# Kernel optimization log

Hardware: AMD Instinct MI355X
Metric: run time of the kernel (lower is better)

The kernel has to match this reference:

```python
import jax, jax.numpy as jnp
import numpy as np

G, N, E = 4, 50000, 800000
F_IN, HID, OUT = 64, 128, 64


def setup_inputs() -> dict:
    key = jax.random.key(0)
    ks = jax.random.split(key, 4)
    x = jax.random.normal(ks[0], (G, N, F_IN), dtype=jnp.float32)
    edge_index = jax.random.randint(ks[1], (G, 2, E), 0, N)
    W1 = jax.random.normal(ks[2], (G, F_IN, HID), dtype=jnp.float32) / np.sqrt(F_IN).astype(np.float32)
    b1 = jnp.zeros((G, HID), dtype=jnp.float32)
    W2 = jax.random.normal(ks[3], (G, HID, OUT), dtype=jnp.float32) / np.sqrt(HID).astype(np.float32)
    b2 = jnp.zeros((G, OUT), dtype=jnp.float32)
    return {"x": x, "edge_index": edge_index, "W1": W1, "b1": b1, "W2": W2, "b2": b2}


def gcn_conv(x, src, dst, W, b):
    # PyG GCNConv: add self loops, symmetric norm D^-1/2 (A+I) D^-1/2, then XW + b
    n = x.shape[0]
    loop = jnp.arange(n)
    s = jnp.concatenate([src, loop])  # [E+N]
    d = jnp.concatenate([dst, loop])
    deg = jax.ops.segment_sum(jnp.ones_like(s, dtype=x.dtype), d, num_segments=n)
    dinv = jax.lax.rsqrt(deg)  # deg >= 1 because of self loops
    norm = dinv[s] * dinv[d]  # [E+N]
    h = x @ W  # [N, F_out]
    msg = h[s] * norm[:, None]  # edge-wise gather (memory-bound)
    out = jax.ops.segment_sum(msg, d, num_segments=n)  # scatter-add
    return out + b


def reference(x, edge_index, W1, b1, W2, b2):
    def per_graph(xg, eg, w1, b1g, w2, b2g):
        src, dst = eg[0], eg[1]
        h = jax.nn.elu(gcn_conv(xg, src, dst, w1, b1g))
        h = jax.nn.elu(gcn_conv(h, src, dst, w2, b2g))
        return h  # [N, OUT]

    out = jax.vmap(per_graph)(x, edge_index, W1, b1, W2, b2)  # [G, N, OUT]
    return out.reshape(G * N, OUT)  # torch.cat over graphs along dim 0
```

## Files before the change

kernel.cpp:

```cpp
#include <hip/hip_runtime.h>
#include <cstdint>

constexpr int G = 4, N = 50000, E = 800000;
constexpr int FIN = 64, HID = 128, FOUT = 64;
constexpr int NB = (N + 1023) / 1024;

constexpr int PB = 64;
constexpr int CP = E / PB;
constexpr int NBK = (N + 255) / 256;

typedef unsigned short ushort;
typedef _Float16 f16;

__device__ __forceinline__ ushort f2h(float f) {
  f16 h = (f16)f;
  return __builtin_bit_cast(ushort, h);
}
__device__ __forceinline__ float h2f(ushort u) {
  f16 h = __builtin_bit_cast(f16, u);
  return (float)h;
}

__device__ __forceinline__ void xcd_map(int b, int& g, int& chunk) {
  int xcd = b & 7;
  int sub = b >> 3;
  g = xcd >> 1;
  chunk = (xcd & 1) * 6250 + sub;
}

__global__ void k_x2h(const float4* __restrict__ X, const float* __restrict__ dinv,
                      ushort4* __restrict__ Xh, int n4) {
  int i = blockIdx.x * blockDim.x + threadIdx.x;
  if (i >= n4) return;
  float sc = dinv[i >> 4];
  float4 v = X[i];
  ushort4 o = {f2h(sc * v.x), f2h(sc * v.y), f2h(sc * v.z), f2h(sc * v.w)};
  Xh[i] = o;
}


__global__ __launch_bounds__(256) void k_phist(const int* __restrict__ ei,
                                               int* __restrict__ PH) {
  __shared__ int h[NBK];
  int pb = blockIdx.x, g = blockIdx.y;
  for (int i = threadIdx.x; i < NBK; i += 256) h[i] = 0;
  __syncthreads();
  const int4* dst4 = (const int4*)(ei + (size_t)g * 2 * E + E + (size_t)pb * CP);
  for (int i = threadIdx.x; i < CP / 4; i += 256) {
    int4 d = dst4[i];
    atomicAdd(&h[d.x >> 8], 1);
    atomicAdd(&h[d.y >> 8], 1);
    atomicAdd(&h[d.z >> 8], 1);
    atomicAdd(&h[d.w >> 8], 1);
  }
  __syncthreads();
  for (int i = threadIdx.x; i < NBK; i += 256)
    PH[((size_t)g * NBK + i) * PB + pb] = h[i];
}

__global__ void k_pscan(const int* __restrict__ PH, int* __restrict__ POFF,
                        int* __restrict__ BB) {
  int g = blockIdx.x, k = threadIdx.x;
  int tot = 0;
  if (k < NBK) {
#pragma unroll 8
    for (int pb = 0; pb < PB; ++pb) tot += PH[((size_t)g * NBK + k) * PB + pb];
  }
  __shared__ int sm[256];
  sm[k] = tot;
  __syncthreads();
  for (int off = 1; off < 256; off <<= 1) {
    int v = (k >= off) ? sm[k - off] : 0;
    __syncthreads();
    sm[k] += v;
    __syncthreads();
  }
  int excl = sm[k] - tot;
  if (k < NBK) {
    BB[g * (NBK + 1) + k] = excl;
    if (k == NBK - 1) BB[g * (NBK + 1) + NBK] = excl + tot;
    int run = excl;
#pragma unroll 8
    for (int pb = 0; pb < PB; ++pb) {
      POFF[((size_t)g * NBK + k) * PB + pb] = run;
      run += PH[((size_t)g * NBK + k) * PB + pb];
    }
  }
}

__global__ __launch_bounds__(256) void k_part(const int* __restrict__ ei,
                                              const int* __restrict__ POFF,
                                              unsigned* __restrict__ pairs) {
  __shared__ int off[NBK];
  __shared__ int rk[NBK];
  int pb = blockIdx.x, g = blockIdx.y;
  for (int i = threadIdx.x; i < NBK; i += 256) {
    off[i] = POFF[((size_t)g * NBK + i) * PB + pb];
    rk[i] = 0;
  }
  __syncthreads();
  const int* base = ei + (size_t)g * 2 * E + (size_t)pb * CP;
  const int4* s4 = (const int4*)base;
  const int4* d4 = (const int4*)(base + E);
  unsigned* pg = pairs + (size_t)g * E;
  for (int i = threadIdx.x; i < CP / 4; i += 256) {
    int4 s = s4[i], d = d4[i];
    int sv[4] = {s.x, s.y, s.z, s.w};
    int dv[4] = {d.x, d.y, d.z, d.w};
#pragma unroll
    for (int k = 0; k < 4; ++k) {
      int b = dv[k] >> 8;
      int r = atomicAdd(&rk[b], 1);
      pg[off[b] + r] = (unsigned)sv[k] | ((unsigned)(dv[k] & 255) << 16);
    }
  }
}

__global__ __launch_bounds__(256) void k_bcnt(const unsigned* __restrict__ pairs,
                                              const int* __restrict__ BB,
                                              int* __restrict__ cnt) {
  __shared__ int h[256];
  int k = blockIdx.x, g = blockIdx.y;
  h[threadIdx.x] = 0;
  __syncthreads();
  int lo = BB[g * (NBK + 1) + k], hi = BB[g * (NBK + 1) + k + 1];
  const unsigned* pg = pairs + (size_t)g * E;
  for (int i = lo + (int)threadIdx.x; i < hi; i += 256)
    atomicAdd(&h[(pg[i] >> 16) & 255], 1);
  __syncthreads();
  int n0 = k << 8;
  int nn = min(256, N - n0);
  if ((int)threadIdx.x < nn) cnt[g * N + n0 + threadIdx.x] = h[threadIdx.x];
}

__global__ __launch_bounds__(256) void k_place(const unsigned* __restrict__ pairs,
                                               const int* __restrict__ BB,
                                               const int* __restrict__ rowptr,
                                               int* __restrict__ col) {
  __shared__ int rp[256];
  __shared__ int rk[256];
  int k = blockIdx.x, g = blockIdx.y;
  int n0 = k << 8;
  int nn = min(256, N - n0);
  if ((int)threadIdx.x < nn) rp[threadIdx.x] = rowptr[g * (N + 1) + n0 + threadIdx.x];
  rk[threadIdx.x] = 0;
  __syncthreads();
  int lo = BB[g * (NBK + 1) + k], hi = BB[g * (NBK + 1) + k + 1];
  const unsigned* pg = pairs + (size_t)g * E;
  int* cg = col + (size_t)g * E;
  for (int i = lo + (int)threadIdx.x; i < hi; i += 256) {
    unsigned p = pg[i];
    int dl = (p >> 16) & 255;
    int r = atomicAdd(&rk[dl], 1);
    cg[rp[dl] + r] = (int)(p & 0xffffu);
  }
}

__global__ void k_scan_partial(const int* __restrict__ cnt, int* __restrict__ part) {
  int g = blockIdx.y, b = blockIdx.x, tid = threadIdx.x;
  int base = b * 1024 + tid * 4;
  int s = 0;
#pragma unroll
  for (int k = 0; k < 4; ++k) {
    int i = base + k;
    if (i < N) s += cnt[g * N + i];
  }
  __shared__ int sm[256];
  sm[tid] = s;
  __syncthreads();
  for (int off = 128; off > 0; off >>= 1) {
    if (tid < off) sm[tid] += sm[tid + off];
    __syncthreads();
  }
  if (tid == 0) part[g * NB + b] = sm[0];
}

__global__ void k_scan_mid(int* __restrict__ part, int* __restrict__ rowptr) {
  int g = blockIdx.x;
  if (threadIdx.x != 0) return;
  int run = 0;
  for (int b = 0; b < NB; ++b) {
    int t = part[g * NB + b];
    part[g * NB + b] = run;
    run += t;
  }
  rowptr[g * (N + 1) + N] = run;
}

__global__ void k_scan_final(const int* __restrict__ cnt, const int* __restrict__ part,
                             int* __restrict__ rowptr, float* __restrict__ dinv) {
  int g = blockIdx.y, b = blockIdx.x, tid = threadIdx.x;
  int base = b * 1024 + tid * 4;
  int c[4];
  int s = 0;
#pragma unroll
  for (int k = 0; k < 4; ++k) {
    int i = base + k;
    c[k] = (i < N) ? cnt[g * N + i] : 0;
    s += c[k];
  }
  __shared__ int sm[256];
  sm[tid] = s;
  __syncthreads();
  for (int off = 1; off < 256; off <<= 1) {
    int v = (tid >= off) ? sm[tid - off] : 0;
    __syncthreads();
    sm[tid] += v;
    __syncthreads();
  }
  int excl = sm[tid] - s + part[g * NB + b];
#pragma unroll
  for (int k = 0; k < 4; ++k) {
    int i = base + k;
    if (i < N) {
      rowptr[g * (N + 1) + i] = excl;
      dinv[g * N + i] = rsqrtf((float)(c[k] + 1));
    }
    excl += c[k];
  }
}

__global__ __launch_bounds__(256) void k_mlp(const float* __restrict__ X,
                                             const float* __restrict__ W1,
                                             const float* __restrict__ b1,
                                             const float* __restrict__ W2,
                                             const float* __restrict__ dinv,
                                             ushort* __restrict__ H2s) {
  constexpr int K = FIN;
  constexpr int PK = K + 1;
  __shared__ float lds[64 * PK];
  ushort* h1s = (ushort*)lds;
  int g = blockIdx.y;
  int R0 = blockIdx.x * 64;
  for (int idx = threadIdx.x; idx < 64 * K; idx += 256) {
    int r = idx >> 6, k = idx & 63;
    int row = R0 + r;
    lds[r * PK + k] = (row < N) ? X[((size_t)g * N + row) * K + k] : 0.f;
  }
  __syncthreads();
  int wv = threadIdx.x >> 6;
  int lane = threadIdx.x & 63;
  int c0 = __builtin_amdgcn_readfirstlane(wv * 32);
  const float* W1g = W1 + (size_t)g * K * HID;
  const float* xrow = &lds[lane * PK];
  float acc[32];
#pragma unroll
  for (int c = 0; c < 32; ++c) acc[c] = 0.f;
#pragma unroll 4
  for (int k = 0; k < K; ++k) {
    float xv = xrow[k];
#pragma unroll
    for (int c = 0; c < 32; ++c)
      acc[c] = fmaf(xv, W1g[(size_t)k * HID + c0 + c], acc[c]);
  }
#pragma unroll
  for (int c = 0; c < 32; ++c) {
    float v = acc[c] + b1[g * HID + c0 + c];
    acc[c] = v > 0.f ? v : expm1f(v);
  }
  __syncthreads();
#pragma unroll
  for (int c2 = 0; c2 < 16; ++c2) {
    unsigned pk = (unsigned)f2h(acc[2 * c2]) | ((unsigned)f2h(acc[2 * c2 + 1]) << 16);
    *(unsigned*)&h1s[lane * 130 + c0 + 2 * c2] = pk;
  }
  __syncthreads();
  int j0 = __builtin_amdgcn_readfirstlane(wv * 16);
  const float* W2g = W2 + (size_t)g * HID * FOUT + j0;
  float acc2[16];
#pragma unroll
  for (int j = 0; j < 16; ++j) acc2[j] = 0.f;
#pragma unroll 4
  for (int c = 0; c < HID; c += 2) {
    unsigned pk = *(const unsigned*)&h1s[lane * 130 + c];
    float f0 = h2f((ushort)(pk & 0xffffu));
    float f1 = h2f((ushort)(pk >> 16));
    const float* w0 = &W2g[(size_t)c * FOUT];
    const float* w1 = &W2g[(size_t)(c + 1) * FOUT];
#pragma unroll
    for (int j = 0; j < 16; ++j) acc2[j] = fmaf(f0, w0[j], acc2[j]);
#pragma unroll
    for (int j = 0; j < 16; ++j) acc2[j] = fmaf(f1, w1[j], acc2[j]);
  }
  int row = R0 + lane;
  if (row < N) {
    float dd = dinv[g * N + row];
    ushort o[16];
#pragma unroll
    for (int j = 0; j < 16; ++j) o[j] = f2h(acc2[j] * dd);
    ushort* dst = H2s + ((size_t)g * N + row) * FOUT + j0;
    *(uint4*)dst = *(uint4*)&o[0];
    *(uint4*)(dst + 8) = *(uint4*)&o[8];
  }
}

__device__ __forceinline__ float agg_row(const ushort* __restrict__ hb,
                                         const int* __restrict__ cl, int rs, int re,
                                         int lane, float acc) {
  int j = rs;
  for (; j + 16 <= re; j += 16) {
    int s[16];
#pragma unroll
    for (int k = 0; k < 16; ++k) s[k] = cl[j + k];
    float v[16];
#pragma unroll
    for (int k = 0; k < 16; ++k) v[k] = h2f(hb[(size_t)s[k] * 64 + lane]);
#pragma unroll
    for (int k = 0; k < 16; ++k) acc += v[k];
  }
  for (; j + 8 <= re; j += 8) {
    int s[8];
#pragma unroll
    for (int k = 0; k < 8; ++k) s[k] = cl[j + k];
    float v[8];
#pragma unroll
    for (int k = 0; k < 8; ++k) v[k] = h2f(hb[(size_t)s[k] * 64 + lane]);
#pragma unroll
    for (int k = 0; k < 8; ++k) acc += v[k];
  }
  for (; j < re; ++j) acc += h2f(hb[(size_t)cl[j] * 64 + lane]);
  return acc;
}

template <int F>
__global__ __launch_bounds__(256) void k_agg_in(const ushort* __restrict__ Xh,
                                                const int* __restrict__ rowptr,
                                                const int* __restrict__ col,
                                                const float* __restrict__ dinv,
                                                float* __restrict__ Z) {
  int g, chunk;
  xcd_map(blockIdx.x, g, chunk);
  int d = __builtin_amdgcn_readfirstlane(chunk * 4 + (threadIdx.x >> 6));
  int lane = threadIdx.x & 63;
  const ushort* hb = Xh + (size_t)g * N * F;
  const int* cl = col + (size_t)g * E;
  int rs = rowptr[g * (N + 1) + d];
  int re = rowptr[g * (N + 1) + d + 1];
  float acc = h2f(hb[(size_t)d * F + lane]);
  acc = agg_row(hb, cl, rs, re, lane, acc);
  Z[((size_t)g * N + d) * F + lane] = dinv[g * N + d] * acc;
}

template <int F>
__global__ __launch_bounds__(256) void k_agg_out(const ushort* __restrict__ Hsrc,
                                                 const int* __restrict__ rowptr,
                                                 const int* __restrict__ col,
                                                 const float* __restrict__ dinv,
                                                 const float* __restrict__ bias,
                                                 float* __restrict__ out) {
  int g, chunk;
  xcd_map(blockIdx.x, g, chunk);
  int d = __builtin_amdgcn_readfirstlane(chunk * 4 + (threadIdx.x >> 6));
  int lane = threadIdx.x & 63;
  const ushort* hb = Hsrc + (size_t)g * N * F;
  const int* cl = col + (size_t)g * E;
  int rs = rowptr[g * (N + 1) + d];
  int re = rowptr[g * (N + 1) + d + 1];
  float acc = h2f(hb[(size_t)d * F + lane]);
  acc = agg_row(hb, cl, rs, re, lane, acc);
  float p = acc * dinv[g * N + d] + bias[g * F + lane];
  p = p > 0.f ? p : expm1f(p);
  out[((size_t)g * N + d) * F + lane] = p;
}

extern "C" void kernel_launch(void* const* d_in, const int* in_sizes, int n_in,
                              void* d_out, int out_size, void* d_ws, size_t ws_size,
                              hipStream_t stream) {
  const float* x = (const float*)d_in[0];
  const int* ei = (const int*)d_in[1];
  const float* W1 = (const float*)d_in[2];
  const float* b1 = (const float*)d_in[3];
  const float* W2 = (const float*)d_in[4];
  const float* b2 = (const float*)d_in[5];
  float* out = (float*)d_out;

  char* p = (char*)d_ws;
  auto alloc = [&](size_t bytes) {
    char* r = p;
    p += (bytes + 255) & ~(size_t)255;
    return r;
  };
  int* cnt = (int*)alloc(sizeof(int) * G * N);
  int* rowptr = (int*)alloc(sizeof(int) * G * (N + 1));
  int* part = (int*)alloc(sizeof(int) * G * NB);
  float* dinv = (float*)alloc(sizeof(float) * G * N);
  int* col = (int*)alloc(sizeof(int) * (size_t)G * E);
  float* z = (float*)alloc(sizeof(float) * (size_t)G * N * FIN);
  char* scratch = (char*)alloc((size_t)103 << 20);
  ushort* h2s = (ushort*)z;
  unsigned* pairs = (unsigned*)scratch;
  int* PH = (int*)(scratch + ((size_t)13 << 20));
  int* POFF = (int*)(scratch + ((size_t)14 << 20));
  int* BB = (int*)(scratch + ((size_t)15 << 20));
  ushort* xh = (ushort*)(scratch + ((size_t)32 << 20));

  k_phist<<<dim3(PB, G), 256, 0, stream>>>(ei, PH);
  k_pscan<<<G, 256, 0, stream>>>(PH, POFF, BB);
  k_part<<<dim3(PB, G), 256, 0, stream>>>(ei, POFF, pairs);
  k_bcnt<<<dim3(NBK, G), 256, 0, stream>>>(pairs, BB, cnt);
  dim3 sg(NB, G);
  k_scan_partial<<<sg, 256, 0, stream>>>(cnt, part);
  k_scan_mid<<<G, 64, 0, stream>>>(part, rowptr);
  k_scan_final<<<sg, 256, 0, stream>>>(cnt, part, rowptr, dinv);
  k_place<<<dim3(NBK, G), 256, 0, stream>>>(pairs, BB, rowptr, col);

  k_x2h<<<(G * N * FIN / 4 + 255) / 256, 256, 0, stream>>>(
      (const float4*)x, dinv, (ushort4*)xh, G * N * FIN / 4);

  k_agg_in<FIN><<<(G * N) / 4, 256, 0, stream>>>(xh, rowptr, col, dinv, z);

  dim3 gg((N + 63) / 64, G);
  k_mlp<<<gg, 256, 0, stream>>>(z, W1, b1, W2, dinv, h2s);

  k_agg_out<FOUT><<<(G * N) / 4, 256, 0, stream>>>(h2s, rowptr, col, dinv, b2, out);
}
```

Baseline: 463.8 us.

## Fuse layer-1 aggregation into the MLP kernel via LDS staging

```diff
diff --git a/kernel.cpp b/kernel.cpp
--- a/kernel.cpp
+++ b/kernel.cpp
@@ -8,6 +8,9 @@
 constexpr int PB = 64;
 constexpr int CP = E / PB;
 constexpr int NBK = (N + 255) / 256;
+
+constexpr int NT = (N + 63) / 64;
+constexpr int NTH = 391;
 
 typedef unsigned short ushort;
 typedef _Float16 f16;
@@ -220,34 +223,76 @@
   }
 }
 
-__global__ __launch_bounds__(256) void k_mlp(const float* __restrict__ X,
-                                             const float* __restrict__ W1,
-                                             const float* __restrict__ b1,
-                                             const float* __restrict__ W2,
-                                             const float* __restrict__ dinv,
-                                             ushort* __restrict__ H2s) {
-  constexpr int K = FIN;
-  constexpr int PK = K + 1;
+__device__ __forceinline__ float agg_row(const ushort* __restrict__ hb,
+                                         const int* __restrict__ cl, int rs, int re,
+                                         int lane, float acc) {
+  int j = rs;
+  for (; j + 16 <= re; j += 16) {
+    int s[16];
+#pragma unroll
+    for (int k = 0; k < 16; ++k) s[k] = cl[j + k];
+    float v[16];
+#pragma unroll
+    for (int k = 0; k < 16; ++k) v[k] = h2f(hb[(size_t)s[k] * 64 + lane]);
+#pragma unroll
+    for (int k = 0; k < 16; ++k) acc += v[k];
+  }
+  for (; j + 8 <= re; j += 8) {
+    int s[8];
+#pragma unroll
+    for (int k = 0; k < 8; ++k) s[k] = cl[j + k];
+    float v[8];
+#pragma unroll
+    for (int k = 0; k < 8; ++k) v[k] = h2f(hb[(size_t)s[k] * 64 + lane]);
+#pragma unroll
+    for (int k = 0; k < 8; ++k) acc += v[k];
+  }
+  for (; j < re; ++j) acc += h2f(hb[(size_t)cl[j] * 64 + lane]);
+  return acc;
+}
+
+__global__ __launch_bounds__(256) void k_l1(const ushort* __restrict__ Xh,
+                                            const int* __restrict__ rowptr,
+                                            const int* __restrict__ col,
+                                            const float* __restrict__ dinv,
+                                            const float* __restrict__ W1,
+                                            const float* __restrict__ b1,
+                                            const float* __restrict__ W2,
+                                            ushort* __restrict__ H2s) {
+  constexpr int PK = FIN + 1;
   __shared__ float lds[64 * PK];
   ushort* h1s = (ushort*)lds;
-  int g = blockIdx.y;
-  int R0 = blockIdx.x * 64;
-  for (int idx = threadIdx.x; idx < 64 * K; idx += 256) {
-    int r = idx >> 6, k = idx & 63;
-    int row = R0 + r;
-    lds[r * PK + k] = (row < N) ? X[((size_t)g * N + row) * K + k] : 0.f;
-  }
-  __syncthreads();
+  int b = blockIdx.x;
+  int xcd = b & 7;
+  int sub = b >> 3;
+  int g = xcd >> 1;
+  int tile = (xcd & 1) * NTH + sub;
+  int R0 = tile * 64;
   int wv = threadIdx.x >> 6;
   int lane = threadIdx.x & 63;
+  const ushort* hb = Xh + (size_t)g * N * FIN;
+  const int* cl = col + (size_t)g * E;
+  for (int i = 0; i < 16; ++i) {
+    int d = __builtin_amdgcn_readfirstlane(R0 + wv * 16 + i);
+    float zv = 0.f;
+    if (d < N) {
+      int rs = rowptr[g * (N + 1) + d];
+      int re = rowptr[g * (N + 1) + d + 1];
+      float acc = h2f(hb[(size_t)d * FIN + lane]);
+      acc = agg_row(hb, cl, rs, re, lane, acc);
+      zv = dinv[g * N + d] * acc;
+    }
+    lds[(wv * 16 + i) * PK + lane] = zv;
+  }
+  __syncthreads();
   int c0 = __builtin_amdgcn_readfirstlane(wv * 32);
-  const float* W1g = W1 + (size_t)g * K * HID;
+  const float* W1g = W1 + (size_t)g * FIN * HID;
   const float* xrow = &lds[lane * PK];
   float acc[32];
 #pragma unroll
   for (int c = 0; c < 32; ++c) acc[c] = 0.f;
 #pragma unroll 4
-  for (int k = 0; k < K; ++k) {
+  for (int k = 0; k < FIN; ++k) {
     float xv = xrow[k];
 #pragma unroll
     for (int c = 0; c < 32; ++c)
@@ -292,53 +337,6 @@
     *(uint4*)dst = *(uint4*)&o[0];
     *(uint4*)(dst + 8) = *(uint4*)&o[8];
   }
-}
-
-__device__ __forceinline__ float agg_row(const ushort* __restrict__ hb,
-                                         const int* __restrict__ cl, int rs, int re,
-                                         int lane, float acc) {
-  int j = rs;
-  for (; j + 16 <= re; j += 16) {
-    int s[16];
-#pragma unroll
-    for (int k = 0; k < 16; ++k) s[k] = cl[j + k];
-    float v[16];
-#pragma unroll
-    for (int k = 0; k < 16; ++k) v[k] = h2f(hb[(size_t)s[k] * 64 + lane]);
-#pragma unroll
-    for (int k = 0; k < 16; ++k) acc += v[k];
-  }
-  for (; j + 8 <= re; j += 8) {
-    int s[8];
-#pragma unroll
-    for (int k = 0; k < 8; ++k) s[k] = cl[j + k];
-    float v[8];
-#pragma unroll
-    for (int k = 0; k < 8; ++k) v[k] = h2f(hb[(size_t)s[k] * 64 + lane]);
-#pragma unroll
-    for (int k = 0; k < 8; ++k) acc += v[k];
-  }
-  for (; j < re; ++j) acc += h2f(hb[(size_t)cl[j] * 64 + lane]);
-  return acc;
-}
-
-template <int F>
-__global__ __launch_bounds__(256) void k_agg_in(const ushort* __restrict__ Xh,
-                                                const int* __restrict__ rowptr,
-                                                const int* __restrict__ col,
-                                                const float* __restrict__ dinv,
-                                                float* __restrict__ Z) {
-  int g, chunk;
-  xcd_map(blockIdx.x, g, chunk);
-  int d = __builtin_amdgcn_readfirstlane(chunk * 4 + (threadIdx.x >> 6));
-  int lane = threadIdx.x & 63;
-  const ushort* hb = Xh + (size_t)g * N * F;
-  const int* cl = col + (size_t)g * E;
-  int rs = rowptr[g * (N + 1) + d];
-  int re = rowptr[g * (N + 1) + d + 1];
-  float acc = h2f(hb[(size_t)d * F + lane]);
-  acc = agg_row(hb, cl, rs, re, lane, acc);
-  Z[((size_t)g * N + d) * F + lane] = dinv[g * N + d] * acc;
 }
 
 template <int F>
@@ -407,10 +405,7 @@
   k_x2h<<<(G * N * FIN / 4 + 255) / 256, 256, 0, stream>>>(
       (const float4*)x, dinv, (ushort4*)xh, G * N * FIN / 4);
 
-  k_agg_in<FIN><<<(G * N) / 4, 256, 0, stream>>>(xh, rowptr, col, dinv, z);
-
-  dim3 gg((N + 63) / 64, G);
-  k_mlp<<<gg, 256, 0, stream>>>(z, W1, b1, W2, dinv, h2s);
+  k_l1<<<8 * NTH, 256, 0, stream>>>(xh, rowptr, col, dinv, W1, b1, W2, h2s);
 
   k_agg_out<FOUT><<<(G * N) / 4, 256, 0, stream>>>(h2s, rowptr, col, dinv, b2, out);
 }
```

After: 445.5 us. 1.04x faster.
